# Kernel optimization log

Measured on AMD Instinct MI355X. Metric: run time of the kernel, lower is better.

Reference implementation:

```python
import jax, jax.numpy as jnp
import numpy as np

B, S, H, I, E, K = 2, 2048, 1024, 2048, 8, 2


def setup_inputs() -> dict:
    key = jax.random.key(0)
    k1, k2, k3, k4, k5 = jax.random.split(key, 5)
    scale_h = 1.0 / np.sqrt(H)
    scale_i = 1.0 / np.sqrt(I)
    return {
        "x": jax.random.normal(k1, (B, S, H), dtype=jnp.float32),
        "Wg": jax.random.normal(k2, (H, E), dtype=jnp.float32) * scale_h,
        "W11": jax.random.normal(k3, (E, H, I), dtype=jnp.float32) * scale_h,
        "W12": jax.random.normal(k4, (E, H, I), dtype=jnp.float32) * scale_h,
        "W2": jax.random.normal(k5, (E, I, H), dtype=jnp.float32) * scale_i,
    }


def reference(x, Wg, W11, W12, W2):
    # Router: softmax over experts, then top-k with renormalization (+1e-8 as in torch ref)
    gate_scores = jax.nn.softmax(x @ Wg, axis=-1)          # [B,S,E]
    topk_scores, topk_idx = jax.lax.top_k(gate_scores, K)   # [B,S,K]
    topk_scores = topk_scores / (topk_scores.sum(-1, keepdims=True) + 1e-8)

    # Dense per-expert SwiGLU on all tokens (matches reference's masked-dense math)
    gate = jnp.einsum('bsh,ehi->bsei', x, W11)              # [B,S,E,I]
    value = jnp.einsum('bsh,ehi->bsei', x, W12)
    fused = (gate * jax.nn.sigmoid(gate)) * value           # SiLU(gate) * value
    expert_out = jnp.einsum('bsei,eih->bseh', fused, W2)    # [B,S,E,H]

    # Gather the top-k experts' outputs per token and combine with routing weights
    gathered = jnp.take_along_axis(expert_out, topk_idx[..., None], axis=2)  # [B,S,K,H]
    out = jnp.sum(topk_scores[..., None] * gathered, axis=2)                 # [B,S,H]
    return out
```

## Files before the change

### kernel.cpp

```cpp
#include <hip/hip_runtime.h>
#include <hip/hip_bf16.h>
#include <stdint.h>

#define B_ 2
#define S_ 2048
#define H_ 1024
#define I_ 2048
#define E_ 8
#define TOK (B_*S_)
#define PAIRS (TOK*2)
#define MAXBLK 80

typedef __bf16 bf16_t;
typedef __bf16 bf16x4 __attribute__((ext_vector_type(4)));
typedef __bf16 bf16x8 __attribute__((ext_vector_type(8)));
typedef float  f32x4  __attribute__((ext_vector_type(4)));
typedef float  f32x16 __attribute__((ext_vector_type(16)));

__device__ __forceinline__ void gl_lds16(const bf16_t* g, bf16_t* l) {
    __builtin_amdgcn_global_load_lds(
        (const __attribute__((address_space(1))) unsigned int*)g,
        (__attribute__((address_space(3))) unsigned int*)l, 16, 0, 0);
}

__global__ void router_kernel(const float* __restrict__ x, const float* __restrict__ Wg,
                              int* __restrict__ top2e, float* __restrict__ top2w,
                              int* __restrict__ counts) {
    int wave = threadIdx.x >> 6;
    int lane = threadIdx.x & 63;
    int t = blockIdx.x * 4 + wave;
    if (t >= TOK) return;
    float acc[E_];
#pragma unroll
    for (int e = 0; e < E_; e++) acc[e] = 0.f;
    const float* xrow = x + (size_t)t * H_;
    for (int j = 0; j < H_ / 64; j++) {
        int h = j * 64 + lane;
        float xv = xrow[h];
        const float4* wg = (const float4*)(Wg + (size_t)h * E_);
        float4 w0 = wg[0], w1 = wg[1];
        acc[0] += xv * w0.x; acc[1] += xv * w0.y; acc[2] += xv * w0.z; acc[3] += xv * w0.w;
        acc[4] += xv * w1.x; acc[5] += xv * w1.y; acc[6] += xv * w1.z; acc[7] += xv * w1.w;
    }
#pragma unroll
    for (int e = 0; e < E_; e++) {
#pragma unroll
        for (int m = 32; m >= 1; m >>= 1) acc[e] += __shfl_xor(acc[e], m, 64);
    }
    if (lane == 0) {
        float mx = acc[0];
        for (int e = 1; e < E_; e++) mx = fmaxf(mx, acc[e]);
        float p[E_]; float z = 0.f;
        for (int e = 0; e < E_; e++) { p[e] = __expf(acc[e] - mx); z += p[e]; }
        for (int e = 0; e < E_; e++) p[e] /= z;
        int i1 = 0; float p1 = p[0];
        for (int e = 1; e < E_; e++) if (p[e] > p1) { p1 = p[e]; i1 = e; }
        int i2 = -1; float p2 = -1.f;
        for (int e = 0; e < E_; e++) if (e != i1 && p[e] > p2) { p2 = p[e]; i2 = e; }
        float s = p1 + p2 + 1e-8f;
        top2e[t * 2]     = i1; top2e[t * 2 + 1] = i2;
        top2w[t * 2]     = p1 / s; top2w[t * 2 + 1] = p2 / s;
        atomicAdd(&counts[i1], 1);
        atomicAdd(&counts[i2], 1);
    }
}

__global__ void scan_kernel(const int* __restrict__ counts, int* __restrict__ offsets,
                            int* __restrict__ cursor, int* __restrict__ blk_e,
                            int* __restrict__ blk_m0, int* __restrict__ nblk) {
    if (threadIdx.x == 0 && blockIdx.x == 0) {
        int run = 0, b = 0;
        for (int e = 0; e < E_; e++) {
            offsets[e] = run; cursor[e] = run;
            int c = counts[e];
            for (int m0 = 0; m0 < c; m0 += 128) { blk_e[b] = e; blk_m0[b] = m0; b++; }
            run += c;
        }
        nblk[0] = b;
    }
}

__global__ void fill_kernel(const int* __restrict__ top2e, const float* __restrict__ top2w,
                            int* __restrict__ cursor, int* __restrict__ pair_tok,
                            float* __restrict__ pair_w) {
    int t = blockIdx.x * blockDim.x + threadIdx.x;
    if (t >= TOK) return;
#pragma unroll
    for (int k = 0; k < 2; k++) {
        int e = top2e[t * 2 + k];
        int pos = atomicAdd(&cursor[e], 1);
        pair_tok[pos] = t;
        pair_w[pos]   = top2w[t * 2 + k];
    }
}

__global__ void castx_kernel(const float* __restrict__ x, bf16_t* __restrict__ xb) {
    size_t i = ((size_t)blockIdx.x * blockDim.x + threadIdx.x) * 4;
    float4 v = *(const float4*)(x + i);
    bf16x4 o = { (bf16_t)v.x, (bf16_t)v.y, (bf16_t)v.z, (bf16_t)v.w };
    *(bf16x4*)(xb + i) = o;
}

__global__ __launch_bounds__(256) void transpose_cast_kernel(
    const float* __restrict__ src, bf16_t* __restrict__ dst, int R, int C) {
    __shared__ float tile[64][65];
    int e = blockIdx.z;
    const float* s = src + (size_t)e * R * C;
    bf16_t* d = dst + (size_t)e * R * C;
    int c0 = blockIdx.x * 64, r0 = blockIdx.y * 64;
    int t = threadIdx.x;
    int lr = t >> 4, lc = (t & 15) * 4;
#pragma unroll
    for (int j = 0; j < 4; j++) {
        int r = r0 + lr + j * 16;
        float4 v = *(const float4*)(s + (size_t)r * C + c0 + lc);
        tile[lr + j * 16][lc + 0] = v.x;
        tile[lr + j * 16][lc + 1] = v.y;
        tile[lr + j * 16][lc + 2] = v.z;
        tile[lr + j * 16][lc + 3] = v.w;
    }
    __syncthreads();
    int oc = t >> 2, os = (t & 3) * 8;
#pragma unroll
    for (int j = 0; j < 2; j++) {
        int base = os + j * 32;
        bf16x8 v;
#pragma unroll
        for (int k = 0; k < 8; k++) v[k] = (bf16_t)tile[base + k][oc];
        *(bf16x8*)(d + (size_t)(c0 + oc) * R + r0 + base) = v;
    }
}

__global__ __launch_bounds__(256, 2) void gemm1_kernel(
    const bf16_t* __restrict__ xb,
    const bf16_t* __restrict__ W11t,
    const bf16_t* __restrict__ W12t,
    const int* __restrict__ counts, const int* __restrict__ offsets,
    const int* __restrict__ blk_e, const int* __restrict__ blk_m0,
    const int* __restrict__ nblk,
    const int* __restrict__ pair_tok,
    bf16_t* __restrict__ fused)
{
    int by = blockIdx.y;
    if (by >= nblk[0]) return;
    int e = blk_e[by];
    int m0 = blk_m0[by];
    int cnt = counts[e];
    int off = offsets[e];
    int n0 = blockIdx.x * 128;

    __shared__ __align__(16) bf16_t la[128 * 64];
    __shared__ __align__(16) bf16_t lb[256 * 64];

    int tid = threadIdx.x;
    int w = tid >> 6, lane = tid & 63;
    int wm = w >> 1, wn = w & 1;
    int lrow = lane >> 3, lcol = lane & 7;
    int scol = lcol ^ lrow;

    const bf16_t* aptr[2];
    const bf16_t* bptr[8];
#pragma unroll
    for (int it = 0; it < 2; it++) {
        ;
    }
    const bf16_t* aptr4[4];
#pragma unroll
    for (int it = 0; it < 4; it++) {
        int r = it * 32 + w * 8 + lrow;
        int grow = m0 + r;
        int tok = pair_tok[off + (grow < cnt ? grow : 0)];
        aptr4[it] = xb + (size_t)tok * H_ + scol * 8;
    }
#pragma unroll
    for (int it = 0; it < 8; it++) {
        int r = it * 32 + w * 8 + lrow;
        const bf16_t* base = (r < 128)
            ? (W11t + ((size_t)e * I_ + n0 + r) * H_)
            : (W12t + ((size_t)e * I_ + n0 + (r - 128)) * H_);
        bptr[it] = base + scol * 8;
    }

    f32x16 acc[2][4];
#pragma unroll
    for (int a = 0; a < 2; a++)
#pragma unroll
        for (int b = 0; b < 4; b++) acc[a][b] = (f32x16)(0.f);

    int r32 = lane & 31;
    int khalf = lane >> 5;
    int rx = r32 & 7;

    for (int k0 = 0; k0 < H_; k0 += 64) {
#pragma unroll
        for (int it = 0; it < 4; it++)
            gl_lds16(aptr4[it] + k0, &la[(it * 32 + w * 8) * 64]);
#pragma unroll
        for (int it = 0; it < 8; it++)
            gl_lds16(bptr[it] + k0, &lb[(it * 32 + w * 8) * 64]);
        __syncthreads();
#pragma unroll
        for (int t16 = 0; t16 < 4; t16++) {
            int seg = t16 * 2 + khalf;
            bf16x8 af[2], bfr[4];
#pragma unroll
            for (int ms = 0; ms < 2; ms++) {
                int row = wm * 64 + ms * 32 + r32;
                af[ms] = *(const bf16x8*)&la[row * 64 + (seg ^ rx) * 8];
            }
#pragma unroll
            for (int ns = 0; ns < 2; ns++) {
                int browg = wn * 64 + ns * 32 + r32;
                bfr[ns]     = *(const bf16x8*)&lb[browg * 64 + (seg ^ rx) * 8];
                bfr[ns + 2] = *(const bf16x8*)&lb[(browg + 128) * 64 + (seg ^ rx) * 8];
            }
#pragma unroll
            for (int ms = 0; ms < 2; ms++)
#pragma unroll
                for (int ns = 0; ns < 4; ns++)
                    acc[ms][ns] = __builtin_amdgcn_mfma_f32_32x32x16_bf16(
                        af[ms], bfr[ns], acc[ms][ns], 0, 0, 0);
        }
        __syncthreads();
    }

#pragma unroll
    for (int ms = 0; ms < 2; ms++) {
#pragma unroll
        for (int ns = 0; ns < 2; ns++) {
            int i = n0 + wn * 64 + ns * 32 + r32;
#pragma unroll
            for (int reg = 0; reg < 16; reg++) {
                int rrow = (reg & 3) + 8 * (reg >> 2) + 4 * khalf;
                int grow = m0 + wm * 64 + ms * 32 + rrow;
                if (grow < cnt) {
                    float g = acc[ms][ns][reg];
                    float v = acc[ms][ns + 2][reg];
                    float f = g * v / (1.f + __expf(-g));
                    fused[(size_t)(off + grow) * I_ + i] = (bf16_t)f;
                }
            }
        }
    }
}

__global__ __launch_bounds__(256, 3) void gemm2_kernel(
    const bf16_t* __restrict__ fused,
    const bf16_t* __restrict__ W2t,
    const int* __restrict__ counts, const int* __restrict__ offsets,
    const int* __restrict__ blk_e, const int* __restrict__ blk_m0,
    const int* __restrict__ nblk,
    const int* __restrict__ pair_tok, const float* __restrict__ pair_w,
    float* __restrict__ out)
{
    int by = blockIdx.y;
    if (by >= nblk[0]) return;
    int e = blk_e[by];
    int m0 = blk_m0[by];
    int cnt = counts[e];
    int off = offsets[e];
    int n0 = blockIdx.x * 128;

    __shared__ __align__(16) bf16_t la[128 * 64];
    __shared__ __align__(16) bf16_t lb[128 * 64];

    int tid = threadIdx.x;
    int w = tid >> 6, lane = tid & 63;
    int wm = w >> 1, wn = w & 1;
    int lrow = lane >> 3, lcol = lane & 7;
    int scol = lcol ^ lrow;

    const bf16_t* aptr[4];
    const bf16_t* bptr[4];
#pragma unroll
    for (int it = 0; it < 4; it++) {
        int r = it * 32 + w * 8 + lrow;
        int grow = m0 + r;
        if (grow >= cnt) grow = cnt - 1;
        aptr[it] = fused + (size_t)(off + grow) * I_ + scol * 8;
        bptr[it] = W2t + ((size_t)e * H_ + n0 + r) * I_ + scol * 8;
    }

    f32x16 acc[2][2];
#pragma unroll
    for (int a = 0; a < 2; a++)
#pragma unroll
        for (int b = 0; b < 2; b++) acc[a][b] = (f32x16)(0.f);

    int r32 = lane & 31;
    int khalf = lane >> 5;
    int rx = r32 & 7;

    for (int k0 = 0; k0 < I_; k0 += 64) {
#pragma unroll
        for (int it = 0; it < 4; it++) {
            gl_lds16(aptr[it] + k0, &la[(it * 32 + w * 8) * 64]);
            gl_lds16(bptr[it] + k0, &lb[(it * 32 + w * 8) * 64]);
        }
        __syncthreads();
#pragma unroll
        for (int t16 = 0; t16 < 4; t16++) {
            int seg = t16 * 2 + khalf;
            bf16x8 af[2], bfr[2];
#pragma unroll
            for (int ms = 0; ms < 2; ms++) {
                int row = wm * 64 + ms * 32 + r32;
                af[ms] = *(const bf16x8*)&la[row * 64 + (seg ^ rx) * 8];
            }
#pragma unroll
            for (int ns = 0; ns < 2; ns++) {
                int brow = wn * 64 + ns * 32 + r32;
                bfr[ns] = *(const bf16x8*)&lb[brow * 64 + (seg ^ rx) * 8];
            }
#pragma unroll
            for (int ms = 0; ms < 2; ms++)
#pragma unroll
                for (int ns = 0; ns < 2; ns++)
                    acc[ms][ns] = __builtin_amdgcn_mfma_f32_32x32x16_bf16(
                        af[ms], bfr[ns], acc[ms][ns], 0, 0, 0);
        }
        __syncthreads();
    }

#pragma unroll
    for (int ms = 0; ms < 2; ms++) {
#pragma unroll
        for (int reg = 0; reg < 16; reg++) {
            int rrow = (reg & 3) + 8 * (reg >> 2) + 4 * khalf;
            int grow = m0 + wm * 64 + ms * 32 + rrow;
            if (grow < cnt) {
                int slot = off + grow;
                int tok = pair_tok[slot];
                float wt = pair_w[slot];
#pragma unroll
                for (int ns = 0; ns < 2; ns++) {
                    int h = n0 + wn * 64 + ns * 32 + r32;
                    atomicAdd(&out[(size_t)tok * H_ + h], wt * acc[ms][ns][reg]);
                }
            }
        }
    }
}

extern "C" void kernel_launch(void* const* d_in, const int* in_sizes, int n_in,
                              void* d_out, int out_size, void* d_ws, size_t ws_size,
                              hipStream_t stream) {
    const float* x   = (const float*)d_in[0];
    const float* Wg  = (const float*)d_in[1];
    const float* W11 = (const float*)d_in[2];
    const float* W12 = (const float*)d_in[3];
    const float* W2  = (const float*)d_in[4];
    float* out = (float*)d_out;

    char* ws = (char*)d_ws;
    size_t o = 0;
    auto alloc = [&](size_t bytes) { size_t r = o; o = (o + bytes + 255) & ~(size_t)255; return r; };
    int*    counts   = (int*)(ws + alloc(E_ * 4));
    int*    offsets  = (int*)(ws + alloc(E_ * 4));
    int*    cursor   = (int*)(ws + alloc(E_ * 4));
    int*    blk_e    = (int*)(ws + alloc(MAXBLK * 4));
    int*    blk_m0   = (int*)(ws + alloc(MAXBLK * 4));
    int*    nblk     = (int*)(ws + alloc(4));
    int*    top2e    = (int*)(ws + alloc(TOK * 2 * 4));
    float*  top2w    = (float*)(ws + alloc(TOK * 2 * 4));
    int*    pair_tok = (int*)(ws + alloc(PAIRS * 4));
    float*  pair_w   = (float*)(ws + alloc(PAIRS * 4));
    bf16_t* xb       = (bf16_t*)(ws + alloc((size_t)TOK * H_ * 2));
    bf16_t* W11t     = (bf16_t*)(ws + alloc((size_t)E_ * I_ * H_ * 2));
    bf16_t* W12t     = (bf16_t*)(ws + alloc((size_t)E_ * I_ * H_ * 2));
    bf16_t* W2t      = (bf16_t*)(ws + alloc((size_t)E_ * I_ * H_ * 2));
    bf16_t* fusedbuf = (bf16_t*)(ws + alloc((size_t)PAIRS * I_ * 2));

    hipMemsetAsync(counts, 0, E_ * 4, stream);
    hipMemsetAsync(d_out, 0, (size_t)out_size * 4, stream);

    router_kernel<<<TOK / 4, 256, 0, stream>>>(x, Wg, top2e, top2w, counts);
    scan_kernel<<<1, 64, 0, stream>>>(counts, offsets, cursor, blk_e, blk_m0, nblk);
    fill_kernel<<<TOK / 256, 256, 0, stream>>>(top2e, top2w, cursor, pair_tok, pair_w);

    castx_kernel<<<(TOK * H_ / 4) / 256, 256, 0, stream>>>(x, xb);
    transpose_cast_kernel<<<dim3(I_ / 64, H_ / 64, E_), 256, 0, stream>>>(W11, W11t, H_, I_);
    transpose_cast_kernel<<<dim3(I_ / 64, H_ / 64, E_), 256, 0, stream>>>(W12, W12t, H_, I_);
    transpose_cast_kernel<<<dim3(H_ / 64, I_ / 64, E_), 256, 0, stream>>>(W2, W2t, I_, H_);

    gemm1_kernel<<<dim3(I_ / 128, MAXBLK), 256, 0, stream>>>(
        xb, W11t, W12t, counts, offsets, blk_e, blk_m0, nblk, pair_tok, fusedbuf);
    gemm2_kernel<<<dim3(H_ / 128, MAXBLK), 256, 0, stream>>>(
        fusedbuf, W2t, counts, offsets, blk_e, blk_m0, nblk, pair_tok, pair_w, out);
}
```

Measured before the change: 541.2 us.

## Replace atomic scatter with per-pair output buffer and combine kernel; widen transpose tiles

gemm2 no longer atomically adds weighted results into the output. It writes each pair's raw result to a per-slot float buffer, and a new combine kernel gathers the two slots per token through an inverse index and applies the routing weights. This drops the output memset and the atomic contention, at the cost of an extra 32MB write/read pass and one more launch. The weight transpose-cast kernel also moves to 64x128 tiles, so each block does more work and fewer blocks are launched.

```diff
diff --git a/kernel.cpp b/kernel.cpp
--- a/kernel.cpp
+++ b/kernel.cpp
@@ -80,9 +80,9 @@
     }
 }
 
-__global__ void fill_kernel(const int* __restrict__ top2e, const float* __restrict__ top2w,
+__global__ void fill_kernel(const int* __restrict__ top2e,
                             int* __restrict__ cursor, int* __restrict__ pair_tok,
-                            float* __restrict__ pair_w) {
+                            int* __restrict__ inv) {
     int t = blockIdx.x * blockDim.x + threadIdx.x;
     if (t >= TOK) return;
 #pragma unroll
@@ -90,7 +90,7 @@
         int e = top2e[t * 2 + k];
         int pos = atomicAdd(&cursor[e], 1);
         pair_tok[pos] = t;
-        pair_w[pos]   = top2w[t * 2 + k];
+        inv[t * 2 + k] = pos;
     }
 }
 
@@ -103,31 +103,33 @@
 
 __global__ __launch_bounds__(256) void transpose_cast_kernel(
     const float* __restrict__ src, bf16_t* __restrict__ dst, int R, int C) {
-    __shared__ float tile[64][65];
+    __shared__ float tile[64][129];
     int e = blockIdx.z;
     const float* s = src + (size_t)e * R * C;
     bf16_t* d = dst + (size_t)e * R * C;
-    int c0 = blockIdx.x * 64, r0 = blockIdx.y * 64;
+    int c0 = blockIdx.x * 128, r0 = blockIdx.y * 64;
     int t = threadIdx.x;
-    int lr = t >> 4, lc = (t & 15) * 4;
+#pragma unroll
+    for (int j = 0; j < 8; j++) {
+        int flat = j * 256 + t;
+        int r = flat >> 5;
+        int c4 = (flat & 31) * 4;
+        float4 v = *(const float4*)(s + (size_t)(r0 + r) * C + c0 + c4);
+        tile[r][c4 + 0] = v.x;
+        tile[r][c4 + 1] = v.y;
+        tile[r][c4 + 2] = v.z;
+        tile[r][c4 + 3] = v.w;
+    }
+    __syncthreads();
 #pragma unroll
     for (int j = 0; j < 4; j++) {
-        int r = r0 + lr + j * 16;
-        float4 v = *(const float4*)(s + (size_t)r * C + c0 + lc);
-        tile[lr + j * 16][lc + 0] = v.x;
-        tile[lr + j * 16][lc + 1] = v.y;
-        tile[lr + j * 16][lc + 2] = v.z;
-        tile[lr + j * 16][lc + 3] = v.w;
-    }
-    __syncthreads();
-    int oc = t >> 2, os = (t & 3) * 8;
-#pragma unroll
-    for (int j = 0; j < 2; j++) {
-        int base = os + j * 32;
+        int flat = j * 256 + t;
+        int orow = flat >> 3;
+        int seg  = (flat & 7) * 8;
         bf16x8 v;
 #pragma unroll
-        for (int k = 0; k < 8; k++) v[k] = (bf16_t)tile[base + k][oc];
-        *(bf16x8*)(d + (size_t)(c0 + oc) * R + r0 + base) = v;
+        for (int k = 0; k < 8; k++) v[k] = (bf16_t)tile[seg + k][orow];
+        *(bf16x8*)(d + (size_t)(c0 + orow) * R + r0 + seg) = v;
     }
 }
 
@@ -158,13 +160,8 @@
     int lrow = lane >> 3, lcol = lane & 7;
     int scol = lcol ^ lrow;
 
-    const bf16_t* aptr[2];
+    const bf16_t* aptr4[4];
     const bf16_t* bptr[8];
-#pragma unroll
-    for (int it = 0; it < 2; it++) {
-        ;
-    }
-    const bf16_t* aptr4[4];
 #pragma unroll
     for (int it = 0; it < 4; it++) {
         int r = it * 32 + w * 8 + lrow;
@@ -250,8 +247,7 @@
     const int* __restrict__ counts, const int* __restrict__ offsets,
     const int* __restrict__ blk_e, const int* __restrict__ blk_m0,
     const int* __restrict__ nblk,
-    const int* __restrict__ pair_tok, const float* __restrict__ pair_w,
-    float* __restrict__ out)
+    float* __restrict__ y)
 {
     int by = blockIdx.y;
     if (by >= nblk[0]) return;
@@ -330,16 +326,27 @@
             int grow = m0 + wm * 64 + ms * 32 + rrow;
             if (grow < cnt) {
                 int slot = off + grow;
-                int tok = pair_tok[slot];
-                float wt = pair_w[slot];
 #pragma unroll
                 for (int ns = 0; ns < 2; ns++) {
                     int h = n0 + wn * 64 + ns * 32 + r32;
-                    atomicAdd(&out[(size_t)tok * H_ + h], wt * acc[ms][ns][reg]);
+                    y[(size_t)slot * H_ + h] = acc[ms][ns][reg];
                 }
             }
         }
     }
+}
+
+__global__ __launch_bounds__(256) void combine_kernel(
+    const float* __restrict__ y, const int* __restrict__ inv,
+    const float* __restrict__ top2w, float* __restrict__ out) {
+    int t = blockIdx.x;
+    int h = threadIdx.x * 4;
+    int s1 = inv[t * 2], s2 = inv[t * 2 + 1];
+    float w1 = top2w[t * 2], w2 = top2w[t * 2 + 1];
+    f32x4 a = *(const f32x4*)(y + (size_t)s1 * H_ + h);
+    f32x4 b = *(const f32x4*)(y + (size_t)s2 * H_ + h);
+    f32x4 r = a * w1 + b * w2;
+    *(f32x4*)(out + (size_t)t * H_ + h) = r;
 }
 
 extern "C" void kernel_launch(void* const* d_in, const int* in_sizes, int n_in,
@@ -364,27 +371,28 @@
     int*    top2e    = (int*)(ws + alloc(TOK * 2 * 4));
     float*  top2w    = (float*)(ws + alloc(TOK * 2 * 4));
     int*    pair_tok = (int*)(ws + alloc(PAIRS * 4));
-    float*  pair_w   = (float*)(ws + alloc(PAIRS * 4));
+    int*    inv      = (int*)(ws + alloc(TOK * 2 * 4));
     bf16_t* xb       = (bf16_t*)(ws + alloc((size_t)TOK * H_ * 2));
     bf16_t* W11t     = (bf16_t*)(ws + alloc((size_t)E_ * I_ * H_ * 2));
     bf16_t* W12t     = (bf16_t*)(ws + alloc((size_t)E_ * I_ * H_ * 2));
     bf16_t* W2t      = (bf16_t*)(ws + alloc((size_t)E_ * I_ * H_ * 2));
     bf16_t* fusedbuf = (bf16_t*)(ws + alloc((size_t)PAIRS * I_ * 2));
+    float*  ybuf     = (float*)(ws + alloc((size_t)PAIRS * H_ * 4));
 
     hipMemsetAsync(counts, 0, E_ * 4, stream);
-    hipMemsetAsync(d_out, 0, (size_t)out_size * 4, stream);
 
     router_kernel<<<TOK / 4, 256, 0, stream>>>(x, Wg, top2e, top2w, counts);
     scan_kernel<<<1, 64, 0, stream>>>(counts, offsets, cursor, blk_e, blk_m0, nblk);
-    fill_kernel<<<TOK / 256, 256, 0, stream>>>(top2e, top2w, cursor, pair_tok, pair_w);
+    fill_kernel<<<TOK / 256, 256, 0, stream>>>(top2e, cursor, pair_tok, inv);
 
     castx_kernel<<<(TOK * H_ / 4) / 256, 256, 0, stream>>>(x, xb);
-    transpose_cast_kernel<<<dim3(I_ / 64, H_ / 64, E_), 256, 0, stream>>>(W11, W11t, H_, I_);
-    transpose_cast_kernel<<<dim3(I_ / 64, H_ / 64, E_), 256, 0, stream>>>(W12, W12t, H_, I_);
-    transpose_cast_kernel<<<dim3(H_ / 64, I_ / 64, E_), 256, 0, stream>>>(W2, W2t, I_, H_);
+    transpose_cast_kernel<<<dim3(I_ / 128, H_ / 64, E_), 256, 0, stream>>>(W11, W11t, H_, I_);
+    transpose_cast_kernel<<<dim3(I_ / 128, H_ / 64, E_), 256, 0, stream>>>(W12, W12t, H_, I_);
+    transpose_cast_kernel<<<dim3(H_ / 128, I_ / 64, E_), 256, 0, stream>>>(W2, W2t, I_, H_);
 
     gemm1_kernel<<<dim3(I_ / 128, MAXBLK), 256, 0, stream>>>(
         xb, W11t, W12t, counts, offsets, blk_e, blk_m0, nblk, pair_tok, fusedbuf);
     gemm2_kernel<<<dim3(H_ / 128, MAXBLK), 256, 0, stream>>>(
-        fusedbuf, W2t, counts, offsets, blk_e, blk_m0, nblk, pair_tok, pair_w, out);
-}
+        fusedbuf, W2t, counts, offsets, blk_e, blk_m0, nblk, ybuf);
+    combine_kernel<<<TOK, 256, 0, stream>>>(ybuf, inv, top2w, out);
+}
```

Result: faster. 527.5 us (-2.5%).
